# Optimization experiments

Measured on AMD Instinct MI355X. Metric: run time of the kernel, lower is better.

Reference implementation:

```python
import jax, jax.numpy as jnp
import numpy as np

N_HEADS = 8
D_HEAD = 64
SCALE = 1.0 / np.sqrt(D_HEAD)  # ProbAttention default scale = 1/sqrt(D)


def setup_inputs() -> dict:
    key = jax.random.key(0)
    ks = jax.random.split(key, 8)
    B, L_dec, L_enc, D = 4, 2048, 2048, 512
    factor = 5
    sample_k = int(factor * np.ceil(np.log(L_enc)))  # 40
    n_top = int(factor * np.ceil(np.log(L_dec)))     # 40
    w = lambda k: jax.random.normal(k, (D, D), jnp.float32) * (1.0 / np.sqrt(D))
    return {
        "x": jax.random.normal(ks[0], (B, L_dec, D), jnp.float32),
        "context": jax.random.normal(ks[1], (B, L_enc, D), jnp.float32),
        "Wq": w(ks[2]), "bq": jnp.zeros((D,), jnp.float32),
        "Wk": w(ks[3]), "bk": jnp.zeros((D,), jnp.float32),
        "Wv": w(ks[4]), "bv": jnp.zeros((D,), jnp.float32),
        "Wo": w(ks[5]), "bo": jnp.zeros((D,), jnp.float32),
        "index_sample": jax.random.randint(ks[6], (L_dec, sample_k), 0, L_enc, jnp.int32),
        "n_top": n_top,
    }


def reference(x, context, Wq, bq, Wk, bk, Wv, bv, Wo, bo, index_sample, n_top):
    B, L_dec, D = x.shape
    L_enc = context.shape[1]
    H, Dh = N_HEADS, D_HEAD
    # QKV projections (torch Linear: y = x @ W.T + b), then [B,H,L,Dh]
    Q = (x @ Wq.T + bq).reshape(B, L_dec, H, Dh).transpose(0, 2, 1, 3)
    K = (context @ Wk.T + bk).reshape(B, L_enc, H, Dh).transpose(0, 2, 1, 3)
    V = (context @ Wv.T + bv).reshape(B, L_enc, H, Dh).transpose(0, 2, 1, 3)
    # --- _prob_QK: sample keys per query, measure sparsity, pick top queries ---
    K_sample = K[:, :, index_sample, :]                    # [B,H,L_dec,sample_k,Dh]
    QK_sample = jnp.einsum('bhld,bhlsd->bhls', Q, K_sample)
    M = QK_sample.max(-1) - QK_sample.sum(-1) / L_enc      # [B,H,L_dec]
    _, top_idx = jax.lax.top_k(M, n_top)                   # [B,H,u]
    Q_red = jnp.take_along_axis(Q, top_idx[..., None], axis=2)  # [B,H,u,Dh]
    scores = jnp.einsum('bhud,bhkd->bhuk', Q_red, K) * SCALE
    # --- initial context: mean of V (mask_flag=False) ---
    ctx = jnp.broadcast_to(V.mean(axis=2, keepdims=True), (B, H, L_dec, Dh))
    # --- update selected query positions with full attention ---
    attn = jax.nn.softmax(scores, axis=-1)
    upd = jnp.einsum('bhuk,bhkd->bhud', attn, V)           # [B,H,u,Dh]
    b_idx = jnp.arange(B)[:, None, None]
    h_idx = jnp.arange(H)[None, :, None]
    ctx = ctx.at[b_idx, h_idx, top_idx].set(upd)
    out = ctx.transpose(0, 2, 1, 3).reshape(B, L_dec, D)
    return out @ Wo.T + bo                                  # dropout = identity (eval)
```

## Files before the change

### kernel.cpp

```cpp
#include <hip/hip_runtime.h>
#include <float.h>

#define BATCH 4
#define LSEQ  2048
#define DMODEL 512
#define NH    8
#define DHD   64
#define NSAMP 40
#define NTOP  40
#define NSEG  16
#define SEGK  128
#define SUBK  64
#define QK_SCALE 0.125f

typedef unsigned short u16;
typedef __attribute__((ext_vector_type(8))) short short8b;
typedef __attribute__((ext_vector_type(4))) float f32x4;
typedef __attribute__((ext_vector_type(4))) float f32x4v;

#define ASTRIDE ((size_t)BATCH * LSEQ * DMODEL)
#define WSTRIDE ((size_t)DMODEL * DMODEL)

static __device__ __forceinline__ u16 f2bf(float x) {
    unsigned u = __float_as_uint(x);
    u += 0x7FFFu + ((u >> 16) & 1u);
    return (u16)(u >> 16);
}
static __device__ __forceinline__ float bf2f(u16 s) {
    return __uint_as_float((unsigned)s << 16);
}
static __device__ __forceinline__ void split2(
    const float4 v, ushort4& o1, ushort4& o2)
{
    const float in[4] = {v.x, v.y, v.z, v.w};
    u16 a[4], b[4];
#pragma unroll
    for (int c = 0; c < 4; ++c) {
        a[c] = f2bf(in[c]);
        b[c] = f2bf(in[c] - bf2f(a[c]));
    }
    o1.x = a[0]; o1.y = a[1]; o1.z = a[2]; o1.w = a[3];
    o2.x = b[0]; o2.y = b[1]; o2.z = b[2]; o2.w = b[3];
}

__global__ __launch_bounds__(256) void split3_all(
    const float* __restrict__ x, const float* __restrict__ ctxin,
    const float* __restrict__ Wq, const float* __restrict__ Wk,
    const float* __restrict__ Wv,
    u16* __restrict__ xsP, u16* __restrict__ csP,
    u16* __restrict__ wqP, u16* __restrict__ wkP, u16* __restrict__ wvP)
{
    const int X4 = 1 << 20;
    const int W4 = 1 << 16;
    const int total = 2 * X4 + 3 * W4;
    for (int i = blockIdx.x * 256 + threadIdx.x; i < total; i += gridDim.x * 256) {
        const float* src; u16* dst; size_t pstride; int i4;
        if (i < X4)            { src = x;     dst = xsP; pstride = ASTRIDE; i4 = i; }
        else if (i < 2 * X4)   { src = ctxin; dst = csP; pstride = ASTRIDE; i4 = i - X4; }
        else {
            const int w = i - 2 * X4;
            const int which = w >> 16, rem = w & (W4 - 1);
            src = (which == 0) ? Wq : (which == 1) ? Wk : Wv;
            dst = (which == 0) ? wqP : (which == 1) ? wkP : wvP;
            pstride = WSTRIDE; i4 = rem;
        }
        const float4 v = reinterpret_cast<const float4*>(src)[i4];
        const float in[4] = {v.x, v.y, v.z, v.w};
        ushort4 o1, o2, o3;
        u16 b1[4], b2[4], b3[4];
#pragma unroll
        for (int c = 0; c < 4; ++c) {
            const float xx = in[c];
            b1[c] = f2bf(xx);
            const float r1 = xx - bf2f(b1[c]);
            b2[c] = f2bf(r1);
            b3[c] = f2bf(r1 - bf2f(b2[c]));
        }
        o1.x = b1[0]; o1.y = b1[1]; o1.z = b1[2]; o1.w = b1[3];
        o2.x = b2[0]; o2.y = b2[1]; o2.z = b2[2]; o2.w = b2[3];
        o3.x = b3[0]; o3.y = b3[1]; o3.z = b3[2]; o3.w = b3[3];
        reinterpret_cast<ushort4*>(dst)[i4]                = o1;
        reinterpret_cast<ushort4*>(dst + pstride)[i4]      = o2;
        reinterpret_cast<ushort4*>(dst + 2 * pstride)[i4]  = o3;
    }
}

template<int NP>
__global__ __launch_bounds__(256) void gemm_mfma(
    const u16* __restrict__ A0, const u16* __restrict__ W0,
    const u16* __restrict__ A1, const u16* __restrict__ W1,
    const float* __restrict__ bias0, const float* __restrict__ bias1,
    float* __restrict__ Out0, float* __restrict__ Out1,
    float* __restrict__ colsum)
{
    const int z = blockIdx.y;
    const int i = blockIdx.x;
    const int xcd = i & 7;
    const int loc = i >> 3;
    const int m0 = (xcd * 8 + (loc & 7)) * 128;
    const int n0 = (loc >> 3) * 128;

    const u16* __restrict__ Ap   = z ? A1 : A0;
    const u16* __restrict__ Wp   = z ? W1 : W0;
    const float* __restrict__ bias = z ? bias1 : bias0;
    float*       __restrict__ Out  = z ? Out1 : Out0;

    __shared__ u16 As[NP][128][40];
    __shared__ u16 Ws[NP][128][40];

    const int tid  = threadIdx.x;
    const int w    = tid >> 6;
    const int lane = tid & 63;
    const int wm   = w >> 1;
    const int wn   = w & 1;
    const int lr   = lane & 15;
    const int lg   = lane >> 4;

    const int srow = tid >> 1;
    const int sc   = (tid & 1) * 16;

    f32x4 acc[4][4];
#pragma unroll
    for (int mf = 0; mf < 4; ++mf)
#pragma unroll
        for (int nf = 0; nf < 4; ++nf)
#pragma unroll
            for (int r = 0; r < 4; ++r) acc[mf][nf][r] = 0.f;

    short8b sa[NP][2], sw[NP][2];
#pragma unroll
    for (int p = 0; p < NP; ++p) {
        const u16* asrc = Ap + p * ASTRIDE + (size_t)(m0 + srow) * DMODEL + sc;
        const u16* wsrc = Wp + p * WSTRIDE + (size_t)(n0 + srow) * DMODEL + sc;
        sa[p][0] = *reinterpret_cast<const short8b*>(asrc);
        sa[p][1] = *reinterpret_cast<const short8b*>(asrc + 8);
        sw[p][0] = *reinterpret_cast<const short8b*>(wsrc);
        sw[p][1] = *reinterpret_cast<const short8b*>(wsrc + 8);
    }

    for (int k0 = 0; k0 < DMODEL; k0 += 32) {
#pragma unroll
        for (int p = 0; p < NP; ++p) {
            *reinterpret_cast<short8b*>(&As[p][srow][sc])     = sa[p][0];
            *reinterpret_cast<short8b*>(&As[p][srow][sc + 8]) = sa[p][1];
            *reinterpret_cast<short8b*>(&Ws[p][srow][sc])     = sw[p][0];
            *reinterpret_cast<short8b*>(&Ws[p][srow][sc + 8]) = sw[p][1];
        }
        __syncthreads();

        if (k0 + 32 < DMODEL) {
#pragma unroll
            for (int p = 0; p < NP; ++p) {
                const u16* asrc =
                    Ap + p * ASTRIDE + (size_t)(m0 + srow) * DMODEL + k0 + 32 + sc;
                const u16* wsrc =
                    Wp + p * WSTRIDE + (size_t)(n0 + srow) * DMODEL + k0 + 32 + sc;
                sa[p][0] = *reinterpret_cast<const short8b*>(asrc);
                sa[p][1] = *reinterpret_cast<const short8b*>(asrc + 8);
                sw[p][0] = *reinterpret_cast<const short8b*>(wsrc);
                sw[p][1] = *reinterpret_cast<const short8b*>(wsrc + 8);
            }
        }

        short8b af[4][NP];
#pragma unroll
        for (int mf = 0; mf < 4; ++mf) {
            const int row = wm * 64 + mf * 16 + lr;
#pragma unroll
            for (int p = 0; p < NP; ++p)
                af[mf][p] = *reinterpret_cast<const short8b*>(&As[p][row][lg * 8]);
        }
#pragma unroll
        for (int nf = 0; nf < 4; ++nf) {
            const int row = wn * 64 + nf * 16 + lr;
            const short8b b1 = *reinterpret_cast<const short8b*>(&Ws[0][row][lg * 8]);
            const short8b b2 = *reinterpret_cast<const short8b*>(&Ws[1][row][lg * 8]);
#pragma unroll
            for (int mf = 0; mf < 4; ++mf) {
                acc[mf][nf] = __builtin_amdgcn_mfma_f32_16x16x32_bf16(af[mf][0], b1, acc[mf][nf], 0, 0, 0);
                acc[mf][nf] = __builtin_amdgcn_mfma_f32_16x16x32_bf16(af[mf][1], b1, acc[mf][nf], 0, 0, 0);
                acc[mf][nf] = __builtin_amdgcn_mfma_f32_16x16x32_bf16(af[mf][0], b2, acc[mf][nf], 0, 0, 0);
                if constexpr (NP == 3) {
                    const short8b b3 = *reinterpret_cast<const short8b*>(&Ws[2][row][lg * 8]);
                    acc[mf][nf] = __builtin_amdgcn_mfma_f32_16x16x32_bf16(af[mf][2], b1, acc[mf][nf], 0, 0, 0);
                    acc[mf][nf] = __builtin_amdgcn_mfma_f32_16x16x32_bf16(af[mf][0], b3, acc[mf][nf], 0, 0, 0);
                    acc[mf][nf] = __builtin_amdgcn_mfma_f32_16x16x32_bf16(af[mf][1], b2, acc[mf][nf], 0, 0, 0);
                }
            }
        }
        __syncthreads();
    }

#pragma unroll
    for (int nf = 0; nf < 4; ++nf) {
        const int n = n0 + wn * 64 + nf * 16 + lr;
        const int h = n >> 6, d = n & 63;
        const float bv_ = bias[n];
        float cs = 0.f;
#pragma unroll
        for (int mf = 0; mf < 4; ++mf) {
#pragma unroll
            for (int r = 0; r < 4; ++r) {
                const int m = m0 + wm * 64 + mf * 16 + lg * 4 + r;
                const int b = m >> 11, l = m & (LSEQ - 1);
                const float val = acc[mf][nf][r] + bv_;
                Out[((size_t)(b * NH + h) * LSEQ + l) * DHD + d] = val;
                cs += val;
            }
        }
        if (colsum)
            atomicAdd(&colsum[((m0 >> 11) * NH + h) * DHD + d], cs);
    }
}

__global__ __launch_bounds__(256) void score_kernel(
    const float* __restrict__ Qt, const float* __restrict__ Kt,
    const int* __restrict__ idxs, float* __restrict__ M,
    unsigned* __restrict__ headmask, float* __restrict__ VmeanRaw,
    float* __restrict__ uacc, float* __restrict__ wsum)
{
    const int flat = blockIdx.x;
    if (flat < 32)        headmask[flat * 256 + threadIdx.x] = 0u;
    else if (flat < 40)   VmeanRaw[(flat - 32) * 256 + threadIdx.x] = 0.f;
    else if (flat < 360)  uacc[(flat - 40) * 256 + threadIdx.x] = 0.f;
    else if (flat < 365) { const int j = (flat - 360) * 256 + threadIdx.x;
                           if (j < NH * BATCH * NTOP) wsum[j] = 0.f; }

    const int xcd  = flat & 7;
    const int slot = flat >> 3;
    const int bh   = xcd * 4 + (slot >> 9);
    const int w    = threadIdx.x >> 6;
    const int lane = threadIdx.x & 63;
    const int l    = (slot & 511) * 4 + w;

    const int g  = lane >> 4;
    const int dl = lane & 15;

#if defined(__has_builtin) && __has_builtin(__builtin_nontemporal_load)
    const f32x4v q4 = __builtin_nontemporal_load(
        reinterpret_cast<const f32x4v*>(Qt + ((size_t)bh * LSEQ + l) * DHD + dl * 4));
#else
    const f32x4v q4 = *reinterpret_cast<const f32x4v*>(
        Qt + ((size_t)bh * LSEQ + l) * DHD + dl * 4);
#endif

    const float* Kb = Kt + (size_t)bh * LSEQ * DHD;
    float vmax = -FLT_MAX, vsum = 0.f;
#pragma unroll
    for (int it = 0; it < 10; ++it) {
        const int s = it * 4 + g;
        const int ks = idxs[l * NSAMP + s];
        const float4 k4 = *reinterpret_cast<const float4*>(
            Kb + (size_t)ks * DHD + dl * 4);
        float p = q4[0] * k4.x + q4[1] * k4.y + q4[2] * k4.z + q4[3] * k4.w;
        p += __shfl_xor(p, 1);
        p += __shfl_xor(p, 2);
        p += __shfl_xor(p, 4);
        p += __shfl_xor(p, 8);
        vmax = fmaxf(vmax, p);
        vsum += p;
    }
    vmax = fmaxf(vmax, __shfl_xor(vmax, 16));
    vsum += __shfl_xor(vsum, 16);
    vmax = fmaxf(vmax, __shfl_xor(vmax, 32));
    vsum += __shfl_xor(vsum, 32);
    if (lane == 0) M[(size_t)bh * LSEQ + l] = vmax - vsum * (1.0f / LSEQ);
}

__global__ __launch_bounds__(256) void topk_kernel(
    const float* __restrict__ M, int* __restrict__ topidx,
    unsigned* __restrict__ headmask, unsigned char* __restrict__ slot)
{
    const int bh = blockIdx.x;
    const int b = bh >> 3, h = bh & 7;
    const int w = threadIdx.x >> 6, lane = threadIdx.x & 63;
    const int base = threadIdx.x * 8;

    float e[8];
    {
        const float4 v0 = *reinterpret_cast<const float4*>(M + (size_t)bh * LSEQ + base);
        const float4 v1 = *reinterpret_cast<const float4*>(M + (size_t)bh * LSEQ + base + 4);
        e[0] = v0.x; e[1] = v0.y; e[2] = v0.z; e[3] = v0.w;
        e[4] = v1.x; e[5] = v1.y; e[6] = v1.z; e[7] = v1.w;
    }

    __shared__ float rv[4];
    __shared__ int   ri[4];
    __shared__ int   winner;

    for (int t = 0; t < NTOP; ++t) {
        float bv = e[0]; int br = 0;
#pragma unroll
        for (int r = 1; r < 8; ++r)
            if (e[r] > bv) { bv = e[r]; br = r; }
        int bi = base + br;
#pragma unroll
        for (int off = 32; off; off >>= 1) {
            const float ov = __shfl_xor(bv, off);
            const int   oi = __shfl_xor(bi, off);
            if (ov > bv || (ov == bv && oi < bi)) { bv = ov; bi = oi; }
        }
        if (lane == 0) { rv[w] = bv; ri[w] = bi; }
        __syncthreads();
        if (threadIdx.x == 0) {
            float fv = rv[0]; int fi = ri[0];
#pragma unroll
            for (int k = 1; k < 4; ++k)
                if (rv[k] > fv || (rv[k] == fv && ri[k] < fi)) { fv = rv[k]; fi = ri[k]; }
            topidx[bh * NTOP + t] = fi;
            atomicOr(&headmask[b * LSEQ + fi], 1u << h);
            slot[bh * LSEQ + fi] = (unsigned char)t;
            winner = fi;
        }
        __syncthreads();
        const int fi = winner;
        if ((fi >> 3) == threadIdx.x) e[fi & 7] = -FLT_MAX;
    }
}

__global__ __launch_bounds__(256) void attn_partial(
    const float* __restrict__ Qt, const float* __restrict__ Kt,
    const float* __restrict__ Vt, const int* __restrict__ topidx,
    float* __restrict__ wsum, float* __restrict__ uacc)
{
    const int bh  = blockIdx.x;
    const int seg = blockIdx.y;
    const int tid = threadIdx.x;
    const int w    = tid >> 6;
    const int lane = tid & 63;
    const int lr = lane & 15, lg = lane >> 4;

    __shared__ u16 Qs[2][48][72];
    __shared__ u16 Ks[2][64][72];
    __shared__ u16 Vtl[2][64][72];
    __shared__ float wsl[48];

    for (int i = tid; i < 48 * 16; i += 256) {
        const int row = i >> 4, c = i & 15;
        float4 v = make_float4(0.f, 0.f, 0.f, 0.f);
        if (row < NTOP) {
            const int l = topidx[bh * NTOP + row];
            v = *reinterpret_cast<const float4*>(
                Qt + ((size_t)bh * LSEQ + l) * DHD + c * 4);
        }
        ushort4 o1, o2;
        split2(v, o1, o2);
        *reinterpret_cast<ushort4*>(&Qs[0][row][c * 4]) = o1;
        *reinterpret_cast<ushort4*>(&Qs[1][row][c * 4]) = o2;
    }
    if (tid < 48) wsl[tid] = 0.f;

    f32x4 pvacc[3];
#pragma unroll
    for (int qt = 0; qt < 3; ++qt)
#pragma unroll
        for (int r = 0; r < 4; ++r) pvacc[qt][r] = 0.f;

    for (int sub = 0; sub < 2; ++sub) {
        const int kbase = seg * SEGK + sub * SUBK;
        __syncthreads();

        for (int i = tid; i < 64 * 16; i += 256) {
            const int key = i >> 4, c = i & 15;
            const size_t g = ((size_t)bh * LSEQ + kbase + key) * DHD + c * 4;
            const float4 kv = *reinterpret_cast<const float4*>(Kt + g);
            const float4 vv = *reinterpret_cast<const float4*>(Vt + g);
            ushort4 k1, k2, v1, v2;
            split2(kv, k1, k2);
            split2(vv, v1, v2);
            *reinterpret_cast<ushort4*>(&Ks[0][key][c * 4]) = k1;
            *reinterpret_cast<ushort4*>(&Ks[1][key][c * 4]) = k2;
            Vtl[0][c * 4 + 0][key] = v1.x; Vtl[0][c * 4 + 1][key] = v1.y;
            Vtl[0][c * 4 + 2][key] = v1.z; Vtl[0][c * 4 + 3][key] = v1.w;
            Vtl[1][c * 4 + 0][key] = v2.x; Vtl[1][c * 4 + 1][key] = v2.y;
            Vtl[1][c * 4 + 2][key] = v2.z; Vtl[1][c * 4 + 3][key] = v2.w;
        }
        __syncthreads();

        f32x4 acc[3];
#pragma unroll
        for (int qt = 0; qt < 3; ++qt)
#pragma unroll
            for (int r = 0; r < 4; ++r) acc[qt][r] = 0.f;
#pragma unroll
        for (int ks = 0; ks < 2; ++ks) {
            const short8b b1 = *reinterpret_cast<const short8b*>(
                &Ks[0][w * 16 + lr][ks * 32 + lg * 8]);
            const short8b b2 = *reinterpret_cast<const short8b*>(
                &Ks[1][w * 16 + lr][ks * 32 + lg * 8]);
#pragma unroll
            for (int qt = 0; qt < 3; ++qt) {
                const short8b a1 = *reinterpret_cast<const short8b*>(
                    &Qs[0][qt * 16 + lr][ks * 32 + lg * 8]);
                const short8b a2 = *reinterpret_cast<const short8b*>(
                    &Qs[1][qt * 16 + lr][ks * 32 + lg * 8]);
                acc[qt] = __builtin_amdgcn_mfma_f32_16x16x32_bf16(a1, b1, acc[qt], 0, 0, 0);
                acc[qt] = __builtin_amdgcn_mfma_f32_16x16x32_bf16(a2, b1, acc[qt], 0, 0, 0);
                acc[qt] = __builtin_amdgcn_mfma_f32_16x16x32_bf16(a1, b2, acc[qt], 0, 0, 0);
            }
        }
        __syncthreads();

#pragma unroll
        for (int qt = 0; qt < 3; ++qt) {
#pragma unroll
            for (int r = 0; r < 4; ++r) {
                const float e = __expf(acc[qt][r] * QK_SCALE);
                float s = e;
                s += __shfl_xor(s, 1);
                s += __shfl_xor(s, 2);
                s += __shfl_xor(s, 4);
                s += __shfl_xor(s, 8);
                const int q = qt * 16 + lg * 4 + r;
                if (lr == 0) atomicAdd(&wsl[q], s);
                const u16 p1 = f2bf(e);
                const u16 p2 = f2bf(e - bf2f(p1));
                Ks[0][q][w * 16 + lr] = p1;
                Ks[1][q][w * 16 + lr] = p2;
            }
        }
        __syncthreads();

#pragma unroll
        for (int ks = 0; ks < 2; ++ks) {
            const short8b b1 = *reinterpret_cast<const short8b*>(
                &Vtl[0][w * 16 + lr][ks * 32 + lg * 8]);
            const short8b b2 = *reinterpret_cast<const short8b*>(
                &Vtl[1][w * 16 + lr][ks * 32 + lg * 8]);
#pragma unroll
            for (int qt = 0; qt < 3; ++qt) {
                const short8b a1 = *reinterpret_cast<const short8b*>(
                    &Ks[0][qt * 16 + lr][ks * 32 + lg * 8]);
                const short8b a2 = *reinterpret_cast<const short8b*>(
                    &Ks[1][qt * 16 + lr][ks * 32 + lg * 8]);
                pvacc[qt] = __builtin_amdgcn_mfma_f32_16x16x32_bf16(a1, b1, pvacc[qt], 0, 0, 0);
                pvacc[qt] = __builtin_amdgcn_mfma_f32_16x16x32_bf16(a2, b1, pvacc[qt], 0, 0, 0);
                pvacc[qt] = __builtin_amdgcn_mfma_f32_16x16x32_bf16(a1, b2, pvacc[qt], 0, 0, 0);
            }
        }
    }

#pragma unroll
    for (int qt = 0; qt < 3; ++qt) {
#pragma unroll
        for (int r = 0; r < 4; ++r) {
            const int q = qt * 16 + lg * 4 + r;
            if (q < NTOP)
                atomicAdd(&uacc[((size_t)bh * NTOP + q) * DHD + w * 16 + lr],
                          pvacc[qt][r]);
        }
    }
    if (tid < NTOP) atomicAdd(&wsum[bh * NTOP + tid], wsl[tid]);
}

__global__ __launch_bounds__(256) void finalize_kernel(
    const float* __restrict__ wsum, const float* __restrict__ uacc,
    const float* __restrict__ VmeanRaw, const float* __restrict__ Wo,
    const float* __restrict__ bo, float* __restrict__ delta,
    float* __restrict__ meanout)
{
    const int blk = blockIdx.x;
    if (blk < 320) {
        const int idx = blk * 256 + threadIdx.x;
        const int bh = idx / 2560;
        const int rem = idx - bh * 2560;
        const int q = rem >> 6, d = rem & 63;
        const float vm = VmeanRaw[bh * DHD + d] * (1.0f / (float)LSEQ);
        delta[idx] = uacc[idx] / wsum[bh * NTOP + q] - vm;
    } else {
        const int b = blk - 320;
        __shared__ float mc[DMODEL];
        for (int i = threadIdx.x; i < DMODEL; i += 256)
            mc[i] = VmeanRaw[b * DMODEL + i] * (1.0f / (float)LSEQ);
        __syncthreads();
        for (int n = threadIdx.x; n < DMODEL; n += 256) {
            float acc = bo[n];
            const float* wr = Wo + (size_t)n * DMODEL;
            for (int k = 0; k < DMODEL; ++k) acc = fmaf(mc[k], wr[k], acc);
            meanout[b * DMODEL + n] = acc;
        }
    }
}

__global__ __launch_bounds__(256) void out_base(
    const float* __restrict__ meanout, float* __restrict__ out)
{
    const int total4 = BATCH * LSEQ * (DMODEL / 4);
    for (int i = blockIdx.x * 256 + threadIdx.x; i < total4; i += gridDim.x * 256) {
        const int row = i >> 7;
        const int b = row >> 11;
        const int c = i & 127;
        reinterpret_cast<float4*>(out)[i] =
            reinterpret_cast<const float4*>(meanout)[b * 128 + c];
    }
}

__global__ __launch_bounds__(128) void out_scatter(
    const int* __restrict__ topidx, const float* __restrict__ delta,
    const float* __restrict__ Wo, float* __restrict__ out)
{
    const int bh = blockIdx.x;
    const int u  = blockIdx.y;
    const int b = bh >> 3, h = bh & 7;
    const int l = topidx[bh * NTOP + u];

    __shared__ float dl[DHD];
    if (threadIdx.x < DHD)
        dl[threadIdx.x] = delta[((size_t)bh * NTOP + u) * DHD + threadIdx.x];
    __syncthreads();

    float* orow = out + ((size_t)b * LSEQ + l) * DMODEL;
#pragma unroll
    for (int c = 0; c < 4; ++c) {
        const int n = threadIdx.x * 4 + c;
        const float4* wr4 = reinterpret_cast<const float4*>(
            Wo + (size_t)n * DMODEL + h * DHD);
        float a = 0.f;
#pragma unroll
        for (int dd = 0; dd < 16; ++dd) {
            const float4 wv = wr4[dd];
            a += dl[dd * 4 + 0] * wv.x + dl[dd * 4 + 1] * wv.y +
                 dl[dd * 4 + 2] * wv.z + dl[dd * 4 + 3] * wv.w;
        }
        atomicAdd(&orow[n], a);
    }
}

extern "C" void kernel_launch(void* const* d_in, const int* in_sizes, int n_in,
                              void* d_out, int out_size, void* d_ws, size_t ws_size,
                              hipStream_t stream)
{
    (void)in_sizes; (void)n_in; (void)out_size; (void)ws_size;
    const float* x     = (const float*)d_in[0];
    const float* ctxin = (const float*)d_in[1];
    const float* Wq    = (const float*)d_in[2];
    const float* bq    = (const float*)d_in[3];
    const float* Wk    = (const float*)d_in[4];
    const float* bk    = (const float*)d_in[5];
    const float* Wv    = (const float*)d_in[6];
    const float* bv    = (const float*)d_in[7];
    const float* Wo    = (const float*)d_in[8];
    const float* bo    = (const float*)d_in[9];
    const int*   idxs  = (const int*)d_in[10];
    float* out = (float*)d_out;

    char* ws = (char*)d_ws;
    size_t off = 0;
    auto alloc = [&](size_t bytes) -> void* {
        void* p = ws + off;
        off += (bytes + 255) & ~(size_t)255;
        return p;
    };

    const size_t qkv_bytes = (size_t)BATCH * NH * LSEQ * DHD * sizeof(float);
    float*         Qt       = (float*)alloc(qkv_bytes);
    float*         Kt       = (float*)alloc(qkv_bytes);
    float*         Vt       = (float*)alloc(qkv_bytes);
    float*         Mbuf     = (float*)alloc((size_t)BATCH * NH * LSEQ * sizeof(float));
    float*         VmeanRaw = (float*)alloc((size_t)BATCH * NH * DHD * sizeof(float));
    float*         meanout  = (float*)alloc((size_t)BATCH * DMODEL * sizeof(float));
    float*         delta    = (float*)alloc((size_t)BATCH * NH * NTOP * DHD * sizeof(float));
    int*           topidx   = (int*)alloc((size_t)BATCH * NH * NTOP * sizeof(int));
    unsigned*      headmask = (unsigned*)alloc((size_t)BATCH * LSEQ * sizeof(unsigned));
    unsigned char* slot     = (unsigned char*)alloc((size_t)BATCH * NH * LSEQ);
    float*         wsum     = (float*)alloc((size_t)BATCH * NH * NTOP * sizeof(float));
    float*         uacc     = (float*)alloc((size_t)BATCH * NH * NTOP * DHD * sizeof(float));
    u16*           xsP      = (u16*)alloc(ASTRIDE * 3 * 2);
    u16*           csP      = (u16*)alloc(ASTRIDE * 3 * 2);
    u16*           wqP      = (u16*)alloc(WSTRIDE * 3 * 2);
    u16*           wkP      = (u16*)alloc(WSTRIDE * 3 * 2);
    u16*           wvP      = (u16*)alloc(WSTRIDE * 3 * 2);

    split3_all<<<2048, 256, 0, stream>>>(x, ctxin, Wq, Wk, Wv,
                                         xsP, csP, wqP, wkP, wvP);

    gemm_mfma<3><<<dim3(256, 2), 256, 0, stream>>>(
        xsP, wqP, csP, wkP, bq, bk, Qt, Kt, nullptr);

    score_kernel<<<(BATCH * NH * LSEQ) / 4, 256, 0, stream>>>(
        Qt, Kt, idxs, Mbuf, headmask, VmeanRaw, uacc, wsum);

    topk_kernel<<<BATCH * NH, 256, 0, stream>>>(Mbuf, topidx, headmask, slot);

    gemm_mfma<2><<<dim3(256, 1), 256, 0, stream>>>(
        csP, wvP, csP, wvP, bv, bv, Vt, Vt, VmeanRaw);

    attn_partial<<<dim3(BATCH * NH, NSEG), 256, 0, stream>>>(
        Qt, Kt, Vt, topidx, wsum, uacc);

    finalize_kernel<<<324, 256, 0, stream>>>(
        wsum, uacc, VmeanRaw, Wo, bo, delta, meanout);

    out_base<<<2048, 256, 0, stream>>>(meanout, out);

    out_scatter<<<dim3(BATCH * NH, NTOP), 128, 0, stream>>>(
        topidx, delta, Wo, out);
}
```

Baseline: 261.3 us.

## Merge Q/K/V GEMMs into one launch and fold small kernels together

Merges the two GEMM launches (3-part Q/K and 2-part V) into a single launch with a z dimension of three, using runtime npl selection so V uses fewer split parts. Moves the zero-initialisation of accumulators into the split kernel and the mean-projection into the topk kernel as extra blocks. Fuses the broadcast base-output fill into the finalize kernel, and removes the unused headmask and slot writes. This cuts launch count and lets V compute alongside Q/K, at the cost of runtime branching in the GEMM inner loop and register and LDS sizing for the 3-part case in every block.

```diff
diff --git a/kernel.cpp b/kernel.cpp
--- a/kernel.cpp
+++ b/kernel.cpp
@@ -48,8 +48,16 @@
     const float* __restrict__ Wq, const float* __restrict__ Wk,
     const float* __restrict__ Wv,
     u16* __restrict__ xsP, u16* __restrict__ csP,
-    u16* __restrict__ wqP, u16* __restrict__ wkP, u16* __restrict__ wvP)
-{
+    u16* __restrict__ wqP, u16* __restrict__ wkP, u16* __restrict__ wvP,
+    float* __restrict__ VmeanRaw, float* __restrict__ uacc,
+    float* __restrict__ wsum)
+{
+    const int flat = blockIdx.x;
+    if (flat < 8)         VmeanRaw[flat * 256 + threadIdx.x] = 0.f;
+    else if (flat < 328)  uacc[(flat - 8) * 256 + threadIdx.x] = 0.f;
+    else if (flat < 333) { const int j = (flat - 328) * 256 + threadIdx.x;
+                           if (j < BATCH * NH * NTOP) wsum[j] = 0.f; }
+
     const int X4 = 1 << 20;
     const int W4 = 1 << 16;
     const int total = 2 * X4 + 3 * W4;
@@ -85,13 +93,14 @@
     }
 }
 
-template<int NP>
-__global__ __launch_bounds__(256) void gemm_mfma(
-    const u16* __restrict__ A0, const u16* __restrict__ W0,
-    const u16* __restrict__ A1, const u16* __restrict__ W1,
-    const float* __restrict__ bias0, const float* __restrict__ bias1,
-    float* __restrict__ Out0, float* __restrict__ Out1,
-    float* __restrict__ colsum)
+__global__ __launch_bounds__(256) void gemm_all(
+    const u16* __restrict__ xsP, const u16* __restrict__ csP,
+    const u16* __restrict__ wqP, const u16* __restrict__ wkP,
+    const u16* __restrict__ wvP,
+    const float* __restrict__ bq, const float* __restrict__ bk,
+    const float* __restrict__ bv,
+    float* __restrict__ Qt, float* __restrict__ Kt, float* __restrict__ Vt,
+    float* __restrict__ VmeanRaw)
 {
     const int z = blockIdx.y;
     const int i = blockIdx.x;
@@ -100,13 +109,14 @@
     const int m0 = (xcd * 8 + (loc & 7)) * 128;
     const int n0 = (loc >> 3) * 128;
 
-    const u16* __restrict__ Ap   = z ? A1 : A0;
-    const u16* __restrict__ Wp   = z ? W1 : W0;
-    const float* __restrict__ bias = z ? bias1 : bias0;
-    float*       __restrict__ Out  = z ? Out1 : Out0;
-
-    __shared__ u16 As[NP][128][40];
-    __shared__ u16 Ws[NP][128][40];
+    const u16* __restrict__ Ap   = (z == 0) ? xsP : csP;
+    const u16* __restrict__ Wp   = (z == 0) ? wqP : (z == 1 ? wkP : wvP);
+    const float* __restrict__ bias = (z == 0) ? bq : (z == 1 ? bk : bv);
+    float*       __restrict__ Out  = (z == 0) ? Qt : (z == 1 ? Kt : Vt);
+    const int npl = (z == 2) ? 2 : 3;
+
+    __shared__ u16 As[3][128][40];
+    __shared__ u16 Ws[3][128][40];
 
     const int tid  = threadIdx.x;
     const int w    = tid >> 6;
@@ -127,48 +137,55 @@
 #pragma unroll
             for (int r = 0; r < 4; ++r) acc[mf][nf][r] = 0.f;
 
-    short8b sa[NP][2], sw[NP][2];
-#pragma unroll
-    for (int p = 0; p < NP; ++p) {
-        const u16* asrc = Ap + p * ASTRIDE + (size_t)(m0 + srow) * DMODEL + sc;
-        const u16* wsrc = Wp + p * WSTRIDE + (size_t)(n0 + srow) * DMODEL + sc;
-        sa[p][0] = *reinterpret_cast<const short8b*>(asrc);
-        sa[p][1] = *reinterpret_cast<const short8b*>(asrc + 8);
-        sw[p][0] = *reinterpret_cast<const short8b*>(wsrc);
-        sw[p][1] = *reinterpret_cast<const short8b*>(wsrc + 8);
+    short8b sa[3][2], sw[3][2];
+#pragma unroll
+    for (int p = 0; p < 3; ++p) {
+        if (p < npl) {
+            const u16* asrc = Ap + p * ASTRIDE + (size_t)(m0 + srow) * DMODEL + sc;
+            const u16* wsrc = Wp + p * WSTRIDE + (size_t)(n0 + srow) * DMODEL + sc;
+            sa[p][0] = *reinterpret_cast<const short8b*>(asrc);
+            sa[p][1] = *reinterpret_cast<const short8b*>(asrc + 8);
+            sw[p][0] = *reinterpret_cast<const short8b*>(wsrc);
+            sw[p][1] = *reinterpret_cast<const short8b*>(wsrc + 8);
+        }
     }
 
     for (int k0 = 0; k0 < DMODEL; k0 += 32) {
 #pragma unroll
-        for (int p = 0; p < NP; ++p) {
-            *reinterpret_cast<short8b*>(&As[p][srow][sc])     = sa[p][0];
-            *reinterpret_cast<short8b*>(&As[p][srow][sc + 8]) = sa[p][1];
-            *reinterpret_cast<short8b*>(&Ws[p][srow][sc])     = sw[p][0];
-            *reinterpret_cast<short8b*>(&Ws[p][srow][sc + 8]) = sw[p][1];
+        for (int p = 0; p < 3; ++p) {
+            if (p < npl) {
+                *reinterpret_cast<short8b*>(&As[p][srow][sc])     = sa[p][0];
+                *reinterpret_cast<short8b*>(&As[p][srow][sc + 8]) = sa[p][1];
+                *reinterpret_cast<short8b*>(&Ws[p][srow][sc])     = sw[p][0];
+                *reinterpret_cast<short8b*>(&Ws[p][srow][sc + 8]) = sw[p][1];
+            }
         }
         __syncthreads();
 
         if (k0 + 32 < DMODEL) {
 #pragma unroll
-            for (int p = 0; p < NP; ++p) {
-                const u16* asrc =
-                    Ap + p * ASTRIDE + (size_t)(m0 + srow) * DMODEL + k0 + 32 + sc;
-                const u16* wsrc =
-                    Wp + p * WSTRIDE + (size_t)(n0 + srow) * DMODEL + k0 + 32 + sc;
-                sa[p][0] = *reinterpret_cast<const short8b*>(asrc);
-                sa[p][1] = *reinterpret_cast<const short8b*>(asrc + 8);
-                sw[p][0] = *reinterpret_cast<const short8b*>(wsrc);
-                sw[p][1] = *reinterpret_cast<const short8b*>(wsrc + 8);
-            }
-        }
-
-        short8b af[4][NP];
+            for (int p = 0; p < 3; ++p) {
+                if (p < npl) {
+                    const u16* asrc =
+                        Ap + p * ASTRIDE + (size_t)(m0 + srow) * DMODEL + k0 + 32 + sc;
+                    const u16* wsrc =
+                        Wp + p * WSTRIDE + (size_t)(n0 + srow) * DMODEL + k0 + 32 + sc;
+                    sa[p][0] = *reinterpret_cast<const short8b*>(asrc);
+                    sa[p][1] = *reinterpret_cast<const short8b*>(asrc + 8);
+                    sw[p][0] = *reinterpret_cast<const short8b*>(wsrc);
+                    sw[p][1] = *reinterpret_cast<const short8b*>(wsrc + 8);
+                }
+            }
+        }
+
+        short8b af[4][3];
 #pragma unroll
         for (int mf = 0; mf < 4; ++mf) {
             const int row = wm * 64 + mf * 16 + lr;
 #pragma unroll
-            for (int p = 0; p < NP; ++p)
-                af[mf][p] = *reinterpret_cast<const short8b*>(&As[p][row][lg * 8]);
+            for (int p = 0; p < 3; ++p)
+                if (p < npl)
+                    af[mf][p] = *reinterpret_cast<const short8b*>(&As[p][row][lg * 8]);
         }
 #pragma unroll
         for (int nf = 0; nf < 4; ++nf) {
@@ -180,8 +197,11 @@
                 acc[mf][nf] = __builtin_amdgcn_mfma_f32_16x16x32_bf16(af[mf][0], b1, acc[mf][nf], 0, 0, 0);
                 acc[mf][nf] = __builtin_amdgcn_mfma_f32_16x16x32_bf16(af[mf][1], b1, acc[mf][nf], 0, 0, 0);
                 acc[mf][nf] = __builtin_amdgcn_mfma_f32_16x16x32_bf16(af[mf][0], b2, acc[mf][nf], 0, 0, 0);
-                if constexpr (NP == 3) {
-                    const short8b b3 = *reinterpret_cast<const short8b*>(&Ws[2][row][lg * 8]);
+            }
+            if (z != 2) {
+                const short8b b3 = *reinterpret_cast<const short8b*>(&Ws[2][row][lg * 8]);
+#pragma unroll
+                for (int mf = 0; mf < 4; ++mf) {
                     acc[mf][nf] = __builtin_amdgcn_mfma_f32_16x16x32_bf16(af[mf][2], b1, acc[mf][nf], 0, 0, 0);
                     acc[mf][nf] = __builtin_amdgcn_mfma_f32_16x16x32_bf16(af[mf][0], b3, acc[mf][nf], 0, 0, 0);
                     acc[mf][nf] = __builtin_amdgcn_mfma_f32_16x16x32_bf16(af[mf][1], b2, acc[mf][nf], 0, 0, 0);
@@ -208,24 +228,16 @@
                 cs += val;
             }
         }
-        if (colsum)
-            atomicAdd(&colsum[((m0 >> 11) * NH + h) * DHD + d], cs);
+        if (z == 2)
+            atomicAdd(&VmeanRaw[((m0 >> 11) * NH + h) * DHD + d], cs);
     }
 }
 
 __global__ __launch_bounds__(256) void score_kernel(
     const float* __restrict__ Qt, const float* __restrict__ Kt,
-    const int* __restrict__ idxs, float* __restrict__ M,
-    unsigned* __restrict__ headmask, float* __restrict__ VmeanRaw,
-    float* __restrict__ uacc, float* __restrict__ wsum)
+    const int* __restrict__ idxs, float* __restrict__ M)
 {
     const int flat = blockIdx.x;
-    if (flat < 32)        headmask[flat * 256 + threadIdx.x] = 0u;
-    else if (flat < 40)   VmeanRaw[(flat - 32) * 256 + threadIdx.x] = 0.f;
-    else if (flat < 360)  uacc[(flat - 40) * 256 + threadIdx.x] = 0.f;
-    else if (flat < 365) { const int j = (flat - 360) * 256 + threadIdx.x;
-                           if (j < NH * BATCH * NTOP) wsum[j] = 0.f; }
-
     const int xcd  = flat & 7;
     const int slot = flat >> 3;
     const int bh   = xcd * 4 + (slot >> 9);
@@ -269,10 +281,26 @@
 
 __global__ __launch_bounds__(256) void topk_kernel(
     const float* __restrict__ M, int* __restrict__ topidx,
-    unsigned* __restrict__ headmask, unsigned char* __restrict__ slot)
+    const float* __restrict__ VmeanRaw, const float* __restrict__ Wo,
+    const float* __restrict__ bo, float* __restrict__ meanout)
 {
     const int bh = blockIdx.x;
-    const int b = bh >> 3, h = bh & 7;
+
+    if (bh >= 32) {
+        const int b = bh - 32;
+        __shared__ float mc[DMODEL];
+        for (int i = threadIdx.x; i < DMODEL; i += 256)
+            mc[i] = VmeanRaw[b * DMODEL + i] * (1.0f / (float)LSEQ);
+        __syncthreads();
+        for (int n = threadIdx.x; n < DMODEL; n += 256) {
+            float acc = bo[n];
+            const float* wr = Wo + (size_t)n * DMODEL;
+            for (int k = 0; k < DMODEL; ++k) acc = fmaf(mc[k], wr[k], acc);
+            meanout[b * DMODEL + n] = acc;
+        }
+        return;
+    }
+
     const int w = threadIdx.x >> 6, lane = threadIdx.x & 63;
     const int base = threadIdx.x * 8;
 
@@ -308,8 +336,6 @@
             for (int k = 1; k < 4; ++k)
                 if (rv[k] > fv || (rv[k] == fv && ri[k] < fi)) { fv = rv[k]; fi = ri[k]; }
             topidx[bh * NTOP + t] = fi;
-            atomicOr(&headmask[b * LSEQ + fi], 1u << h);
-            slot[bh * LSEQ + fi] = (unsigned char)t;
             winner = fi;
         }
         __syncthreads();
@@ -453,11 +479,10 @@
     if (tid < NTOP) atomicAdd(&wsum[bh * NTOP + tid], wsl[tid]);
 }
 
-__global__ __launch_bounds__(256) void finalize_kernel(
+__global__ __launch_bounds__(256) void finalize_base(
     const float* __restrict__ wsum, const float* __restrict__ uacc,
-    const float* __restrict__ VmeanRaw, const float* __restrict__ Wo,
-    const float* __restrict__ bo, float* __restrict__ delta,
-    float* __restrict__ meanout)
+    const float* __restrict__ VmeanRaw, const float* __restrict__ meanout,
+    float* __restrict__ delta, float* __restrict__ out)
 {
     const int blk = blockIdx.x;
     if (blk < 320) {
@@ -468,30 +493,14 @@
         const float vm = VmeanRaw[bh * DHD + d] * (1.0f / (float)LSEQ);
         delta[idx] = uacc[idx] / wsum[bh * NTOP + q] - vm;
     } else {
-        const int b = blk - 320;
-        __shared__ float mc[DMODEL];
-        for (int i = threadIdx.x; i < DMODEL; i += 256)
-            mc[i] = VmeanRaw[b * DMODEL + i] * (1.0f / (float)LSEQ);
-        __syncthreads();
-        for (int n = threadIdx.x; n < DMODEL; n += 256) {
-            float acc = bo[n];
-            const float* wr = Wo + (size_t)n * DMODEL;
-            for (int k = 0; k < DMODEL; ++k) acc = fmaf(mc[k], wr[k], acc);
-            meanout[b * DMODEL + n] = acc;
-        }
-    }
-}
-
-__global__ __launch_bounds__(256) void out_base(
-    const float* __restrict__ meanout, float* __restrict__ out)
-{
-    const int total4 = BATCH * LSEQ * (DMODEL / 4);
-    for (int i = blockIdx.x * 256 + threadIdx.x; i < total4; i += gridDim.x * 256) {
-        const int row = i >> 7;
-        const int b = row >> 11;
-        const int c = i & 127;
-        reinterpret_cast<float4*>(out)[i] =
-            reinterpret_cast<const float4*>(meanout)[b * 128 + c];
+        const int total4 = BATCH * LSEQ * (DMODEL / 4);
+        for (int i = (blk - 320) * 256 + threadIdx.x; i < total4; i += 2048 * 256) {
+            const int row = i >> 7;
+            const int b = row >> 11;
+            const int c = i & 127;
+            reinterpret_cast<float4*>(out)[i] =
+                reinterpret_cast<const float4*>(meanout)[b * 128 + c];
+        }
     }
 }
 
@@ -561,8 +570,6 @@
     float*         meanout  = (float*)alloc((size_t)BATCH * DMODEL * sizeof(float));
     float*         delta    = (float*)alloc((size_t)BATCH * NH * NTOP * DHD * sizeof(float));
     int*           topidx   = (int*)alloc((size_t)BATCH * NH * NTOP * sizeof(int));
-    unsigned*      headmask = (unsigned*)alloc((size_t)BATCH * LSEQ * sizeof(unsigned));
-    unsigned char* slot     = (unsigned char*)alloc((size_t)BATCH * NH * LSEQ);
     float*         wsum     = (float*)alloc((size_t)BATCH * NH * NTOP * sizeof(float));
     float*         uacc     = (float*)alloc((size_t)BATCH * NH * NTOP * DHD * sizeof(float));
     u16*           xsP      = (u16*)alloc(ASTRIDE * 3 * 2);
@@ -572,26 +579,23 @@
     u16*           wvP      = (u16*)alloc(WSTRIDE * 3 * 2);
 
     split3_all<<<2048, 256, 0, stream>>>(x, ctxin, Wq, Wk, Wv,
-                                         xsP, csP, wqP, wkP, wvP);
-
-    gemm_mfma<3><<<dim3(256, 2), 256, 0, stream>>>(
-        xsP, wqP, csP, wkP, bq, bk, Qt, Kt, nullptr);
+                                         xsP, csP, wqP, wkP, wvP,
+                                         VmeanRaw, uacc, wsum);
+
+    gemm_all<<<dim3(256, 3), 256, 0, stream>>>(
+        xsP, csP, wqP, wkP, wvP, bq, bk, bv, Qt, Kt, Vt, VmeanRaw);
 
     score_kernel<<<(BATCH * NH * LSEQ) / 4, 256, 0, stream>>>(
-        Qt, Kt, idxs, Mbuf, headmask, VmeanRaw, uacc, wsum);
-
-    topk_kernel<<<BATCH * NH, 256, 0, stream>>>(Mbuf, topidx, headmask, slot);
-
-    gemm_mfma<2><<<dim3(256, 1), 256, 0, stream>>>(
-        csP, wvP, csP, wvP, bv, bv, Vt, Vt, VmeanRaw);
+        Qt, Kt, idxs, Mbuf);
+
+    topk_kernel<<<36, 256, 0, stream>>>(
+        Mbuf, topidx, VmeanRaw, Wo, bo, meanout);
 
     attn_partial<<<dim3(BATCH * NH, NSEG), 256, 0, stream>>>(
         Qt, Kt, Vt, topidx, wsum, uacc);
 
-    finalize_kernel<<<324, 256, 0, stream>>>(
-        wsum, uacc, VmeanRaw, Wo, bo, delta, meanout);
-
-    out_base<<<2048, 256, 0, stream>>>(meanout, out);
+    finalize_base<<<2368, 256, 0, stream>>>(
+        wsum, uacc, VmeanRaw, meanout, delta, out);
 
     out_scatter<<<dim3(BATCH * NH, NTOP), 128, 0, stream>>>(
         topidx, delta, Wo, out);
```

Result: faster. 224.6 us (-14.1%).
